# Optimization experiments

Measured on AMD Instinct MI355X. Metric: run time of the kernel, lower is better.

## Reference

```python
import jax, jax.numpy as jnp
import numpy as np

EPS = 1e-8
TEMP = 1.0
NUM_SUPERPIXEL = 2048
NUM_SMALL = 8192  # args.small_nseg


def setup_inputs() -> dict:
    key = jax.random.key(0)
    ks = jax.random.split(key, 9)
    N, C, H, W = 4, 19, 512, 512
    S, Ssm = NUM_SUPERPIXEL, NUM_SMALL
    return {
        "inputs": jax.random.normal(ks[0], (N, C, H, W), jnp.float32),
        "inputs_weak": jax.random.normal(ks[1], (N, C, H, W), jnp.float32),
        "targets": jax.random.bernoulli(ks[2], 0.1, (N, S, C + 1)).astype(jnp.float32),
        "spmasks": jax.random.bernoulli(ks[3], 0.8, (N, H, W)),
        "spmasks_weak": jax.random.bernoulli(ks[4], 0.8, (N, H, W)),
        "superpixels": jax.random.randint(ks[5], (N, H, W), 0, S, jnp.int32),
        "superpixels_weak": jax.random.randint(ks[6], (N, H, W), 0, S, jnp.int32),
        "superpixel_smalls": jax.random.randint(ks[7], (N, H, W), 0, Ssm, jnp.int32),
        "spx_smalls_weak": jax.random.randint(ks[8], (N, H, W), 0, Ssm, jnp.int32),
    }


def _per_sample(out_w, seg_w_raw, mask_w, small_w, trg, nll, seg_s_raw, mask_s):
    # out_w: [HWo, C] weak softmax; nll: [HW, C] strong -log softmax
    HWo, C = out_w.shape
    S, Ssm = NUM_SUPERPIXEL, NUM_SMALL
    # route invalid weak pixels to dummy segment S (mimics boolean compaction)
    seg_w = jnp.where(mask_w, seg_w_raw, S)
    max_v = jax.ops.segment_max(out_w, seg_w, num_segments=S + 1)  # [S+1, C]
    pix = jnp.arange(HWo, dtype=jnp.int32)[:, None]
    cand = jnp.where(out_w == max_v[seg_w], pix, HWo)
    idx = jax.ops.segment_min(cand, seg_w, num_segments=S + 1)[:S]  # [S, C] argmax pixel per (sp, class)
    has_pixel = idx[:, 0] < HWo  # superpixel received >=1 valid pixel (scatter_max OOR filter)
    sel_small = small_w[jnp.clip(idx, 0, HWo - 1)]  # [S, C] small-spx id of per-class argmax pixel
    pair = has_pixel[:, None] & (trg > 0)  # selected (superpixel, class) pairs
    # strong branch: per-small-superpixel NLL sum + pixel counts
    seg_s = jnp.where(mask_s, seg_s_raw, Ssm)
    sumpool = jax.ops.segment_sum(nll, seg_s, num_segments=Ssm + 1)[:Ssm]  # [Ssm, C]
    counts = jax.ops.segment_sum(mask_s.astype(jnp.int32), seg_s, num_segments=Ssm + 1)[:Ssm]  # [Ssm]
    val = sumpool[sel_small, jnp.arange(C)[None, :]]  # [S, C]
    sz = counts[sel_small]  # [S, C]
    loss_i = jnp.sum(jnp.where(pair, val, 0.0))
    nv_i = jnp.sum(jnp.where(pair, sz, 0))
    return loss_i, nv_i


def reference(inputs, inputs_weak, targets, spmasks, spmasks_weak,
              superpixels, superpixels_weak, superpixel_smalls, spx_smalls_weak):
    N, C, H, W = inputs.shape
    out_w = jax.nn.softmax(inputs_weak / TEMP, axis=1).transpose(0, 2, 3, 1).reshape(N, -1, C)
    out_s = jax.nn.softmax(inputs / TEMP, axis=1).transpose(0, 2, 3, 1).reshape(N, -1, C)
    nll = -jnp.log(out_s + EPS)
    loss_i, nv_i = jax.vmap(_per_sample)(
        out_w,
        superpixels_weak.reshape(N, -1),
        spmasks_weak.reshape(N, -1),
        spx_smalls_weak.reshape(N, -1),
        targets[..., :-1],
        nll,
        superpixel_smalls.reshape(N, -1),
        spmasks.reshape(N, -1),
    )
    num_valid = 1 + jnp.sum(nv_i)
    return jnp.sum(loss_i) / num_valid.astype(jnp.float32)
```

## Files before the change

kernel.cpp:

```cpp
#include <hip/hip_runtime.h>

constexpr int kN = 4, kC = 19, kH = 512, kW = 512;
constexpr int kHW = kH * kW;
constexpr int kS = 2048;
constexpr int kSsm = 8192;
constexpr float kEps = 1e-8f;

constexpr int kNSC = kN * kS * kC;
constexpr int kCombineBlocks = (kNSC + 255) / 256;

constexpr size_t OFF_AMAX = 0;
constexpr size_t SZ_AMAX  = (size_t)kN * kS * kC * 8;
constexpr size_t OFF_SUM  = OFF_AMAX + SZ_AMAX;
constexpr size_t SZ_SUM   = (size_t)kN * kSsm * kC * 4;
constexpr size_t OFF_CNT  = OFF_SUM + SZ_SUM;
constexpr size_t SZ_CNT   = (size_t)kN * kSsm * 4;
constexpr size_t OFF_TM   = OFF_CNT + SZ_CNT;
constexpr size_t SZ_TM    = (size_t)kN * kS * 4;
constexpr size_t OFF_NM   = OFF_TM + SZ_TM;
constexpr size_t SZ_NM    = (size_t)kN * kSsm * 4;
constexpr size_t OFF_PL   = OFF_NM + SZ_NM;
constexpr size_t SZ_PL    = (size_t)kCombineBlocks * 4;
constexpr size_t OFF_PN   = OFF_PL + SZ_PL;
constexpr size_t SZ_PN    = (size_t)kCombineBlocks * 4;
constexpr size_t WS_TOTAL = OFF_PN + SZ_PN;

__global__ void tmask_kernel(const float* __restrict__ targets,
                             unsigned* __restrict__ tmask) {
    int gid = blockIdx.x * blockDim.x + threadIdx.x;
    if (gid >= kN * kS) return;
    const float* t = targets + (size_t)gid * (kC + 1);
    unsigned m = 0;
#pragma unroll
    for (int c = 0; c < kC; ++c)
        if (t[c] > 0.f) m |= (1u << c);
    tmask[gid] = m;
}

__global__ void weak_argmax_kernel(const float* __restrict__ logits,
                                   const unsigned char* __restrict__ mask,
                                   const int* __restrict__ seg,
                                   const unsigned* __restrict__ tmask,
                                   unsigned long long* __restrict__ amax) {
    int gid = blockIdx.x * blockDim.x + threadIdx.x;
    if (gid >= kN * kHW) return;
    if (!mask[gid]) return;
    int n = gid / kHW;
    int p = gid - n * kHW;
    int s = seg[gid];
    unsigned tm = tmask[n * kS + s];
    if (!tm) return;

    const float* base = logits + (size_t)n * kC * kHW + p;
    float x[kC];
    float m = -1e30f;
#pragma unroll
    for (int c = 0; c < kC; ++c) {
        x[c] = base[(size_t)c * kHW];
        m = fmaxf(m, x[c]);
    }
    float sum = 0.f;
#pragma unroll
    for (int c = 0; c < kC; ++c) {
        x[c] = expf(x[c] - m);
        sum += x[c];
    }
    float inv = 1.f / sum;

    unsigned long long lowbits = (unsigned int)(~(unsigned int)p);
    unsigned long long* dst = amax + ((size_t)n * kS + s) * kC;
#pragma unroll
    for (int c = 0; c < kC; ++c) {
        if (tm & (1u << c)) {
            float v = x[c] * inv;
            unsigned long long key =
                ((unsigned long long)__float_as_uint(v) << 32) | lowbits;
            atomicMax(&dst[c], key);
        }
    }
}

__global__ void need_mark_kernel(const unsigned long long* __restrict__ amax,
                                 const unsigned* __restrict__ tmask,
                                 const int* __restrict__ small_w,
                                 unsigned* __restrict__ needmask) {
    int gid = blockIdx.x * blockDim.x + threadIdx.x;
    if (gid >= kNSC) return;
    int n = gid / (kS * kC);
    int rem = gid - n * (kS * kC);
    int s = rem / kC;
    int c = rem - s * kC;
    if (!((tmask[n * kS + s] >> c) & 1u)) return;
    unsigned long long packed = amax[gid];
    if (packed == 0ULL) return;
    unsigned pix = ~(unsigned)(packed & 0xFFFFFFFFULL);
    int sel = small_w[(size_t)n * kHW + pix];
    atomicOr(&needmask[n * kSsm + sel], 1u << c);
}

__global__ void strong_sumpool_kernel(const float* __restrict__ logits,
                                      const unsigned char* __restrict__ mask,
                                      const int* __restrict__ seg,
                                      const unsigned* __restrict__ needmask,
                                      float* __restrict__ sumpool,
                                      int* __restrict__ counts) {
    int gid = blockIdx.x * blockDim.x + threadIdx.x;
    if (gid >= kN * kHW) return;
    if (!mask[gid]) return;
    int n = gid / kHW;
    int p = gid - n * kHW;
    int ss = seg[gid];
    unsigned nm = needmask[n * kSsm + ss];
    if (!nm) return;

    const float* base = logits + (size_t)n * kC * kHW + p;
    float x[kC];
    float m = -1e30f;
#pragma unroll
    for (int c = 0; c < kC; ++c) {
        x[c] = base[(size_t)c * kHW];
        m = fmaxf(m, x[c]);
    }
    float sum = 0.f;
#pragma unroll
    for (int c = 0; c < kC; ++c) {
        x[c] = expf(x[c] - m);
        sum += x[c];
    }
    float inv = 1.f / sum;

    float* dst = sumpool + ((size_t)n * kSsm + ss) * kC;
#pragma unroll
    for (int c = 0; c < kC; ++c) {
        if (nm & (1u << c)) {
            float nll = -logf(x[c] * inv + kEps);
            atomicAdd(&dst[c], nll);
        }
    }
    atomicAdd(&counts[n * kSsm + ss], 1);
}

__global__ void combine_kernel(const unsigned long long* __restrict__ amax,
                               const unsigned* __restrict__ tmask,
                               const int* __restrict__ small_w,
                               const float* __restrict__ sumpool,
                               const int* __restrict__ counts,
                               float* __restrict__ ploss,
                               int* __restrict__ pnv) {
    __shared__ float sLoss[4];
    __shared__ int sNv[4];
    int gid = blockIdx.x * blockDim.x + threadIdx.x;
    float lv = 0.f;
    int nvv = 0;
    if (gid < kNSC) {
        int n = gid / (kS * kC);
        int rem = gid - n * (kS * kC);
        int s = rem / kC;
        int c = rem - s * kC;
        if ((tmask[n * kS + s] >> c) & 1u) {
            unsigned long long packed = amax[gid];
            if (packed != 0ULL) {
                unsigned pix = ~(unsigned)(packed & 0xFFFFFFFFULL);
                int sel = small_w[(size_t)n * kHW + pix];
                lv = sumpool[((size_t)n * kSsm + sel) * kC + c];
                nvv = counts[n * kSsm + sel];
            }
        }
    }
#pragma unroll
    for (int off = 32; off > 0; off >>= 1) {
        lv += __shfl_down(lv, off);
        nvv += __shfl_down(nvv, off);
    }
    int wave = threadIdx.x >> 6;
    if ((threadIdx.x & 63) == 0) {
        sLoss[wave] = lv;
        sNv[wave] = nvv;
    }
    __syncthreads();
    if (threadIdx.x == 0) {
        float tl = sLoss[0] + sLoss[1] + sLoss[2] + sLoss[3];
        int tn = sNv[0] + sNv[1] + sNv[2] + sNv[3];
        ploss[blockIdx.x] = tl;
        pnv[blockIdx.x] = tn;
    }
}

__global__ void finalize_kernel(const float* __restrict__ ploss,
                                const int* __restrict__ pnv,
                                float* __restrict__ out) {
    __shared__ float sLoss[4];
    __shared__ int sNv[4];
    float lv = 0.f;
    int nvv = 0;
    for (int i = threadIdx.x; i < kCombineBlocks; i += 256) {
        lv += ploss[i];
        nvv += pnv[i];
    }
#pragma unroll
    for (int off = 32; off > 0; off >>= 1) {
        lv += __shfl_down(lv, off);
        nvv += __shfl_down(nvv, off);
    }
    int wave = threadIdx.x >> 6;
    if ((threadIdx.x & 63) == 0) {
        sLoss[wave] = lv;
        sNv[wave] = nvv;
    }
    __syncthreads();
    if (threadIdx.x == 0) {
        float tl = sLoss[0] + sLoss[1] + sLoss[2] + sLoss[3];
        int tn = sNv[0] + sNv[1] + sNv[2] + sNv[3];
        out[0] = tl / (float)(1 + tn);
    }
}

extern "C" void kernel_launch(void* const* d_in, const int* in_sizes, int n_in,
                              void* d_out, int out_size, void* d_ws, size_t ws_size,
                              hipStream_t stream) {
    const float* inputs            = (const float*)d_in[0];
    const float* inputs_weak       = (const float*)d_in[1];
    const float* targets           = (const float*)d_in[2];
    const unsigned char* spmasks      = (const unsigned char*)d_in[3];
    const unsigned char* spmasks_weak = (const unsigned char*)d_in[4];
    const int* superpixels_weak    = (const int*)d_in[6];
    const int* superpixel_smalls   = (const int*)d_in[7];
    const int* spx_smalls_weak     = (const int*)d_in[8];
    float* out = (float*)d_out;

    unsigned long long* amax = (unsigned long long*)((char*)d_ws + OFF_AMAX);
    float* sumpool           = (float*)((char*)d_ws + OFF_SUM);
    int* counts              = (int*)((char*)d_ws + OFF_CNT);
    unsigned* tmask          = (unsigned*)((char*)d_ws + OFF_TM);
    unsigned* needmask       = (unsigned*)((char*)d_ws + OFF_NM);
    float* ploss             = (float*)((char*)d_ws + OFF_PL);
    int* pnv                 = (int*)((char*)d_ws + OFF_PN);

    hipMemsetAsync(d_ws, 0, WS_TOTAL, stream);

    int pixTotal = kN * kHW;
    int pixBlocks = (pixTotal + 255) / 256;

    tmask_kernel<<<(kN * kS + 255) / 256, 256, 0, stream>>>(targets, tmask);
    weak_argmax_kernel<<<pixBlocks, 256, 0, stream>>>(inputs_weak, spmasks_weak,
                                                      superpixels_weak, tmask, amax);
    need_mark_kernel<<<kCombineBlocks, 256, 0, stream>>>(amax, tmask, spx_smalls_weak,
                                                         needmask);
    strong_sumpool_kernel<<<pixBlocks, 256, 0, stream>>>(inputs, spmasks,
                                                         superpixel_smalls,
                                                         needmask, sumpool, counts);
    combine_kernel<<<kCombineBlocks, 256, 0, stream>>>(amax, tmask, spx_smalls_weak,
                                                       sumpool, counts, ploss, pnv);
    finalize_kernel<<<1, 256, 0, stream>>>(ploss, pnv, out);
}
```

Before: 67.64 us.

## Fuse memset into init, process two pixels per thread, fold finalize into combine

```diff
diff --git a/kernel.cpp b/kernel.cpp
--- a/kernel.cpp
+++ b/kernel.cpp
@@ -7,7 +7,7 @@
 constexpr float kEps = 1e-8f;
 
 constexpr int kNSC = kN * kS * kC;
-constexpr int kCombineBlocks = (kNSC + 255) / 256;
+constexpr int kCombineBlocks = 64;
 
 constexpr size_t OFF_AMAX = 0;
 constexpr size_t SZ_AMAX  = (size_t)kN * kS * kC * 8;
@@ -15,26 +15,33 @@
 constexpr size_t SZ_SUM   = (size_t)kN * kSsm * kC * 4;
 constexpr size_t OFF_CNT  = OFF_SUM + SZ_SUM;
 constexpr size_t SZ_CNT   = (size_t)kN * kSsm * 4;
-constexpr size_t OFF_TM   = OFF_CNT + SZ_CNT;
+constexpr size_t OFF_NM   = OFF_CNT + SZ_CNT;
+constexpr size_t SZ_NM    = (size_t)kN * kSsm * 4;
+constexpr size_t OFF_TK   = OFF_NM + SZ_NM;
+constexpr size_t SZ_TK    = 16;
+constexpr size_t ZERO_BYTES = OFF_TK + SZ_TK;
+constexpr size_t ZERO_CHUNKS = ZERO_BYTES / 16;
+constexpr size_t OFF_TM   = ZERO_BYTES;
 constexpr size_t SZ_TM    = (size_t)kN * kS * 4;
-constexpr size_t OFF_NM   = OFF_TM + SZ_TM;
-constexpr size_t SZ_NM    = (size_t)kN * kSsm * 4;
-constexpr size_t OFF_PL   = OFF_NM + SZ_NM;
+constexpr size_t OFF_PL   = OFF_TM + SZ_TM;
 constexpr size_t SZ_PL    = (size_t)kCombineBlocks * 4;
 constexpr size_t OFF_PN   = OFF_PL + SZ_PL;
 constexpr size_t SZ_PN    = (size_t)kCombineBlocks * 4;
 constexpr size_t WS_TOTAL = OFF_PN + SZ_PN;
 
-__global__ void tmask_kernel(const float* __restrict__ targets,
-                             unsigned* __restrict__ tmask) {
-    int gid = blockIdx.x * blockDim.x + threadIdx.x;
-    if (gid >= kN * kS) return;
-    const float* t = targets + (size_t)gid * (kC + 1);
-    unsigned m = 0;
-#pragma unroll
-    for (int c = 0; c < kC; ++c)
-        if (t[c] > 0.f) m |= (1u << c);
-    tmask[gid] = m;
+__global__ void init_kernel(const float* __restrict__ targets,
+                            unsigned* __restrict__ tmask,
+                            ulong2* __restrict__ ws) {
+    size_t gid = (size_t)blockIdx.x * blockDim.x + threadIdx.x;
+    if (gid < ZERO_CHUNKS) ws[gid] = ulong2{0ULL, 0ULL};
+    if (gid < (size_t)kN * kS) {
+        const float* t = targets + gid * (kC + 1);
+        unsigned m = 0;
+#pragma unroll
+        for (int c = 0; c < kC; ++c)
+            if (t[c] > 0.f) m |= (1u << c);
+        tmask[gid] = m;
+    }
 }
 
 __global__ void weak_argmax_kernel(const float* __restrict__ logits,
@@ -42,40 +49,52 @@
                                    const int* __restrict__ seg,
                                    const unsigned* __restrict__ tmask,
                                    unsigned long long* __restrict__ amax) {
-    int gid = blockIdx.x * blockDim.x + threadIdx.x;
-    if (gid >= kN * kHW) return;
-    if (!mask[gid]) return;
-    int n = gid / kHW;
-    int p = gid - n * kHW;
-    int s = seg[gid];
-    unsigned tm = tmask[n * kS + s];
-    if (!tm) return;
+    int t = blockIdx.x * blockDim.x + threadIdx.x;
+    if (t >= kN * kHW / 2) return;
+    int n = t / (kHW / 2);
+    int p = (t - n * (kHW / 2)) * 2;
+    int pixbase = n * kHW + p;
+
+    uchar2 mk = *(const uchar2*)&mask[pixbase];
+    int2 sg = *(const int2*)&seg[pixbase];
+    unsigned tm0 = mk.x ? tmask[n * kS + sg.x] : 0u;
+    unsigned tm1 = mk.y ? tmask[n * kS + sg.y] : 0u;
+    if (!(tm0 | tm1)) return;
 
     const float* base = logits + (size_t)n * kC * kHW + p;
-    float x[kC];
-    float m = -1e30f;
-#pragma unroll
-    for (int c = 0; c < kC; ++c) {
-        x[c] = base[(size_t)c * kHW];
-        m = fmaxf(m, x[c]);
-    }
-    float sum = 0.f;
-#pragma unroll
-    for (int c = 0; c < kC; ++c) {
-        x[c] = expf(x[c] - m);
-        sum += x[c];
-    }
-    float inv = 1.f / sum;
-
-    unsigned long long lowbits = (unsigned int)(~(unsigned int)p);
-    unsigned long long* dst = amax + ((size_t)n * kS + s) * kC;
-#pragma unroll
-    for (int c = 0; c < kC; ++c) {
-        if (tm & (1u << c)) {
-            float v = x[c] * inv;
+    float2 x[kC];
+    float m0 = -1e30f, m1 = -1e30f;
+#pragma unroll
+    for (int c = 0; c < kC; ++c) {
+        x[c] = *(const float2*)&base[(size_t)c * kHW];
+        m0 = fmaxf(m0, x[c].x);
+        m1 = fmaxf(m1, x[c].y);
+    }
+    float s0 = 0.f, s1 = 0.f;
+#pragma unroll
+    for (int c = 0; c < kC; ++c) {
+        x[c].x = expf(x[c].x - m0);
+        x[c].y = expf(x[c].y - m1);
+        s0 += x[c].x;
+        s1 += x[c].y;
+    }
+    float inv0 = 1.f / s0, inv1 = 1.f / s1;
+
+    unsigned long long lo0 = (unsigned)~(unsigned)p;
+    unsigned long long lo1 = (unsigned)~(unsigned)(p + 1);
+    unsigned long long* dst0 = amax + ((size_t)n * kS + sg.x) * kC;
+    unsigned long long* dst1 = amax + ((size_t)n * kS + sg.y) * kC;
+#pragma unroll
+    for (int c = 0; c < kC; ++c) {
+        if ((tm0 >> c) & 1u) {
             unsigned long long key =
-                ((unsigned long long)__float_as_uint(v) << 32) | lowbits;
-            atomicMax(&dst[c], key);
+                ((unsigned long long)__float_as_uint(x[c].x * inv0) << 32) | lo0;
+            atomicMax(&dst0[c], key);
+        }
+        if ((tm1 >> c) & 1u) {
+            unsigned long long key =
+                ((unsigned long long)__float_as_uint(x[c].y * inv1) << 32) | lo1;
+            atomicMax(&dst1[c], key);
         }
     }
 }
@@ -104,40 +123,48 @@
                                       const unsigned* __restrict__ needmask,
                                       float* __restrict__ sumpool,
                                       int* __restrict__ counts) {
-    int gid = blockIdx.x * blockDim.x + threadIdx.x;
-    if (gid >= kN * kHW) return;
-    if (!mask[gid]) return;
-    int n = gid / kHW;
-    int p = gid - n * kHW;
-    int ss = seg[gid];
-    unsigned nm = needmask[n * kSsm + ss];
-    if (!nm) return;
+    int t = blockIdx.x * blockDim.x + threadIdx.x;
+    if (t >= kN * kHW / 2) return;
+    int n = t / (kHW / 2);
+    int p = (t - n * (kHW / 2)) * 2;
+    int pixbase = n * kHW + p;
+
+    uchar2 mk = *(const uchar2*)&mask[pixbase];
+    int2 sg = *(const int2*)&seg[pixbase];
+    unsigned nm0 = mk.x ? needmask[n * kSsm + sg.x] : 0u;
+    unsigned nm1 = mk.y ? needmask[n * kSsm + sg.y] : 0u;
+    if (!(nm0 | nm1)) return;
 
     const float* base = logits + (size_t)n * kC * kHW + p;
-    float x[kC];
-    float m = -1e30f;
-#pragma unroll
-    for (int c = 0; c < kC; ++c) {
-        x[c] = base[(size_t)c * kHW];
-        m = fmaxf(m, x[c]);
-    }
-    float sum = 0.f;
-#pragma unroll
-    for (int c = 0; c < kC; ++c) {
-        x[c] = expf(x[c] - m);
-        sum += x[c];
-    }
-    float inv = 1.f / sum;
-
-    float* dst = sumpool + ((size_t)n * kSsm + ss) * kC;
-#pragma unroll
-    for (int c = 0; c < kC; ++c) {
-        if (nm & (1u << c)) {
-            float nll = -logf(x[c] * inv + kEps);
-            atomicAdd(&dst[c], nll);
-        }
-    }
-    atomicAdd(&counts[n * kSsm + ss], 1);
+    float2 x[kC];
+    float m0 = -1e30f, m1 = -1e30f;
+#pragma unroll
+    for (int c = 0; c < kC; ++c) {
+        x[c] = *(const float2*)&base[(size_t)c * kHW];
+        m0 = fmaxf(m0, x[c].x);
+        m1 = fmaxf(m1, x[c].y);
+    }
+    float s0 = 0.f, s1 = 0.f;
+#pragma unroll
+    for (int c = 0; c < kC; ++c) {
+        x[c].x = expf(x[c].x - m0);
+        x[c].y = expf(x[c].y - m1);
+        s0 += x[c].x;
+        s1 += x[c].y;
+    }
+    float inv0 = 1.f / s0, inv1 = 1.f / s1;
+
+    float* dst0 = sumpool + ((size_t)n * kSsm + sg.x) * kC;
+    float* dst1 = sumpool + ((size_t)n * kSsm + sg.y) * kC;
+#pragma unroll
+    for (int c = 0; c < kC; ++c) {
+        if ((nm0 >> c) & 1u)
+            atomicAdd(&dst0[c], -logf(x[c].x * inv0 + kEps));
+        if ((nm1 >> c) & 1u)
+            atomicAdd(&dst1[c], -logf(x[c].y * inv1 + kEps));
+    }
+    if (nm0) atomicAdd(&counts[n * kSsm + sg.x], 1);
+    if (nm1) atomicAdd(&counts[n * kSsm + sg.y], 1);
 }
 
 __global__ void combine_kernel(const unsigned long long* __restrict__ amax,
@@ -146,26 +173,27 @@
                                const float* __restrict__ sumpool,
                                const int* __restrict__ counts,
                                float* __restrict__ ploss,
-                               int* __restrict__ pnv) {
+                               int* __restrict__ pnv,
+                               unsigned* __restrict__ ticket,
+                               float* __restrict__ out) {
     __shared__ float sLoss[4];
     __shared__ int sNv[4];
-    int gid = blockIdx.x * blockDim.x + threadIdx.x;
+    __shared__ bool amLast;
     float lv = 0.f;
     int nvv = 0;
-    if (gid < kNSC) {
+    for (int gid = blockIdx.x * blockDim.x + threadIdx.x; gid < kNSC;
+         gid += kCombineBlocks * 256) {
         int n = gid / (kS * kC);
         int rem = gid - n * (kS * kC);
         int s = rem / kC;
         int c = rem - s * kC;
-        if ((tmask[n * kS + s] >> c) & 1u) {
-            unsigned long long packed = amax[gid];
-            if (packed != 0ULL) {
-                unsigned pix = ~(unsigned)(packed & 0xFFFFFFFFULL);
-                int sel = small_w[(size_t)n * kHW + pix];
-                lv = sumpool[((size_t)n * kSsm + sel) * kC + c];
-                nvv = counts[n * kSsm + sel];
-            }
-        }
+        if (!((tmask[n * kS + s] >> c) & 1u)) continue;
+        unsigned long long packed = amax[gid];
+        if (packed == 0ULL) continue;
+        unsigned pix = ~(unsigned)(packed & 0xFFFFFFFFULL);
+        int sel = small_w[(size_t)n * kHW + pix];
+        lv += sumpool[((size_t)n * kSsm + sel) * kC + c];
+        nvv += counts[n * kSsm + sel];
     }
 #pragma unroll
     for (int off = 32; off > 0; off >>= 1) {
@@ -179,39 +207,29 @@
     }
     __syncthreads();
     if (threadIdx.x == 0) {
-        float tl = sLoss[0] + sLoss[1] + sLoss[2] + sLoss[3];
-        int tn = sNv[0] + sNv[1] + sNv[2] + sNv[3];
-        ploss[blockIdx.x] = tl;
-        pnv[blockIdx.x] = tn;
-    }
-}
-
-__global__ void finalize_kernel(const float* __restrict__ ploss,
-                                const int* __restrict__ pnv,
-                                float* __restrict__ out) {
-    __shared__ float sLoss[4];
-    __shared__ int sNv[4];
-    float lv = 0.f;
-    int nvv = 0;
-    for (int i = threadIdx.x; i < kCombineBlocks; i += 256) {
-        lv += ploss[i];
-        nvv += pnv[i];
-    }
-#pragma unroll
-    for (int off = 32; off > 0; off >>= 1) {
-        lv += __shfl_down(lv, off);
-        nvv += __shfl_down(nvv, off);
-    }
-    int wave = threadIdx.x >> 6;
-    if ((threadIdx.x & 63) == 0) {
-        sLoss[wave] = lv;
-        sNv[wave] = nvv;
+        ploss[blockIdx.x] = sLoss[0] + sLoss[1] + sLoss[2] + sLoss[3];
+        pnv[blockIdx.x]   = sNv[0] + sNv[1] + sNv[2] + sNv[3];
+        __threadfence();
+        unsigned prev = atomicAdd(ticket, 1u);
+        amLast = (prev == kCombineBlocks - 1);
     }
     __syncthreads();
-    if (threadIdx.x == 0) {
-        float tl = sLoss[0] + sLoss[1] + sLoss[2] + sLoss[3];
-        int tn = sNv[0] + sNv[1] + sNv[2] + sNv[3];
-        out[0] = tl / (float)(1 + tn);
+    if (amLast) {
+        __threadfence();
+        float tl = 0.f;
+        int tn = 0;
+        if (threadIdx.x < kCombineBlocks) {
+            tl = ((volatile float*)ploss)[threadIdx.x];
+            tn = ((volatile int*)pnv)[threadIdx.x];
+        }
+        if (threadIdx.x < 64) {
+#pragma unroll
+            for (int off = 32; off > 0; off >>= 1) {
+                tl += __shfl_down(tl, off);
+                tn += __shfl_down(tn, off);
+            }
+            if (threadIdx.x == 0) out[0] = tl / (float)(1 + tn);
+        }
     }
 }
 
@@ -231,25 +249,25 @@
     unsigned long long* amax = (unsigned long long*)((char*)d_ws + OFF_AMAX);
     float* sumpool           = (float*)((char*)d_ws + OFF_SUM);
     int* counts              = (int*)((char*)d_ws + OFF_CNT);
+    unsigned* needmask       = (unsigned*)((char*)d_ws + OFF_NM);
+    unsigned* ticket         = (unsigned*)((char*)d_ws + OFF_TK);
     unsigned* tmask          = (unsigned*)((char*)d_ws + OFF_TM);
-    unsigned* needmask       = (unsigned*)((char*)d_ws + OFF_NM);
     float* ploss             = (float*)((char*)d_ws + OFF_PL);
     int* pnv                 = (int*)((char*)d_ws + OFF_PN);
 
-    hipMemsetAsync(d_ws, 0, WS_TOTAL, stream);
-
-    int pixTotal = kN * kHW;
-    int pixBlocks = (pixTotal + 255) / 256;
-
-    tmask_kernel<<<(kN * kS + 255) / 256, 256, 0, stream>>>(targets, tmask);
-    weak_argmax_kernel<<<pixBlocks, 256, 0, stream>>>(inputs_weak, spmasks_weak,
-                                                      superpixels_weak, tmask, amax);
-    need_mark_kernel<<<kCombineBlocks, 256, 0, stream>>>(amax, tmask, spx_smalls_weak,
-                                                         needmask);
-    strong_sumpool_kernel<<<pixBlocks, 256, 0, stream>>>(inputs, spmasks,
-                                                         superpixel_smalls,
-                                                         needmask, sumpool, counts);
+    int initThreads = (int)ZERO_CHUNKS;
+    init_kernel<<<(initThreads + 255) / 256, 256, 0, stream>>>(targets, tmask,
+                                                               (ulong2*)d_ws);
+    int pairTotal = kN * kHW / 2;
+    int pairBlocks = (pairTotal + 255) / 256;
+    weak_argmax_kernel<<<pairBlocks, 256, 0, stream>>>(inputs_weak, spmasks_weak,
+                                                       superpixels_weak, tmask, amax);
+    need_mark_kernel<<<(kNSC + 255) / 256, 256, 0, stream>>>(amax, tmask,
+                                                             spx_smalls_weak, needmask);
+    strong_sumpool_kernel<<<pairBlocks, 256, 0, stream>>>(inputs, spmasks,
+                                                          superpixel_smalls,
+                                                          needmask, sumpool, counts);
     combine_kernel<<<kCombineBlocks, 256, 0, stream>>>(amax, tmask, spx_smalls_weak,
-                                                       sumpool, counts, ploss, pnv);
-    finalize_kernel<<<1, 256, 0, stream>>>(ploss, pnv, out);
-}
+                                                       sumpool, counts, ploss, pnv,
+                                                       ticket, out);
+}
```

Measured after the change: 75.63 us. +11.8%, slower.
